# Performance work log

Measured on AMD Instinct MI355X. Metric: run time of the kernel, lower is better.

Reference implementation:

```python
import jax, jax.numpy as jnp
import numpy as np

NUM_HEADS = 16
HEAD_DIM = 64  # hidden 1024 / 16 heads


def setup_inputs() -> dict:
    key = jax.random.key(0)
    ks = jax.random.split(key, 7)
    B, S, D = 16, 1024, 1024
    scale = 1.0 / np.sqrt(D)
    return {
        "hidden_states": jax.random.normal(ks[0], (B, S, D), dtype=jnp.float32),
        "Wq": jax.random.normal(ks[1], (D, D), dtype=jnp.float32) * scale,
        "bq": jax.random.normal(ks[2], (D,), dtype=jnp.float32) * 0.01,
        "Wk": jax.random.normal(ks[3], (D, D), dtype=jnp.float32) * scale,
        "bk": jax.random.normal(ks[4], (D,), dtype=jnp.float32) * 0.01,
        "Wv": jax.random.normal(ks[5], (D, D), dtype=jnp.float32) * scale,
        "bv": jax.random.normal(ks[6], (D,), dtype=jnp.float32) * 0.01,
    }


def _split_heads(x):
    # [B, S, H*Dh] -> [B, H, S, Dh]
    B, S, _ = x.shape
    return x.reshape(B, S, NUM_HEADS, HEAD_DIM).transpose(0, 2, 1, 3)


def reference(hidden_states, Wq, bq, Wk, bk, Wv, bv):
    # Linear layers use torch convention: y = x @ W^T + b
    q = _split_heads(hidden_states @ Wq.T + bq)  # [B,H,S,Dh]
    k = _split_heads(hidden_states @ Wk.T + bk)
    v = _split_heads(hidden_states @ Wv.T + bv)

    scores = jnp.einsum("bhqd,bhkd->bhqk", q, k) / jnp.sqrt(
        jnp.asarray(HEAD_DIM, dtype=q.dtype)
    )
    probs = jax.nn.softmax(scores, axis=-1)  # dropout is identity at eval
    ctx = jnp.einsum("bhqk,bhkd->bhqd", probs, v)  # [B,H,S,Dh]
    B, H, S, Dh = ctx.shape
    return ctx.transpose(0, 2, 1, 3).reshape(B, S, H * Dh)
```

## Files before the change

kernel.cpp:

```cpp
#include <hip/hip_runtime.h>
#include <hip/hip_bf16.h>
#include <cstdint>
#include <math.h>

typedef __bf16 bf16;
typedef __bf16 bf16x8 __attribute__((ext_vector_type(8)));
typedef __bf16 bf16x4 __attribute__((ext_vector_type(4)));
typedef float  f32x4  __attribute__((ext_vector_type(4)));
typedef float  f32x16 __attribute__((ext_vector_type(16)));

#define B_  16
#define S_  1024
#define D_  1024
#define H_  16
#define DH_ 64

__device__ __forceinline__ bf16x8 ld8f(const float* __restrict__ p) {
    f32x4 a = *(const f32x4*)p;
    f32x4 b = *(const f32x4*)(p + 4);
    bf16x8 r;
    r[0] = (bf16)a[0]; r[1] = (bf16)a[1]; r[2] = (bf16)a[2]; r[3] = (bf16)a[3];
    r[4] = (bf16)b[0]; r[5] = (bf16)b[1]; r[6] = (bf16)b[2]; r[7] = (bf16)b[3];
    return r;
}
__device__ __forceinline__ float clampf(float x) {
    return fminf(fmaxf(x, -1e4f), 1e4f);
}
__device__ __forceinline__ void async_ld16(const void* g, void* l) {
    __builtin_amdgcn_global_load_lds(
        (const __attribute__((address_space(1))) void*)(uintptr_t)g,
        (__attribute__((address_space(3))) void*)(uint32_t)(uintptr_t)l,
        16, 0, 0);
}

#define CVT_CHUNKS 2490368u
#define CVT_THREADS 622592u
extern "C" __global__ __launch_bounds__(256)
void cvt_all(const float* __restrict__ X,  const float* __restrict__ Wq,
             const float* __restrict__ Wk, const float* __restrict__ Wv,
             bf16* __restrict__ Xb, bf16* __restrict__ Wb)
{
    const size_t NX = (size_t)B_ * S_ * D_;
    const size_t NW = (size_t)D_ * D_;
    uint32_t tid = blockIdx.x * 256 + threadIdx.x;
    #pragma unroll
    for (int j = 0; j < 4; j++) {
        size_t base = ((size_t)tid + (size_t)j * CVT_THREADS) * 8;
        const float* src; bf16* dst;
        if (base < NX) { src = X + base; dst = Xb + base; }
        else {
            size_t r = base - NX;
            int wsel = (int)(r / NW);
            size_t off = r - (size_t)wsel * NW;
            src = (wsel == 0 ? Wq : (wsel == 1 ? Wk : Wv)) + off;
            dst = Wb + r;
        }
        *(bf16x8*)dst = ld8f(src);
    }
}

extern "C" __global__ __launch_bounds__(512, 2)
void qkv_gemm_bf16(const bf16* __restrict__ Xb, const bf16* __restrict__ Wb,
                   const float* __restrict__ bq, const float* __restrict__ bk,
                   const float* __restrict__ bv,
                   bf16* __restrict__ Qo, bf16* __restrict__ Ko, bf16* __restrict__ Vo)
{
    __shared__ __align__(16) char smem[131072];

    const int t    = threadIdx.x;
    const int w    = t >> 6;
    const int lane = t & 63;
    const int fr   = lane & 15;
    const int fg   = lane >> 4;
    const int wr   = w >> 2;
    const int wn   = w & 3;

    const int id     = blockIdx.x;
    const int l      = id >> 3;
    const int tile_n = l >> 3;
    const int tile_m = (id & 7) * 8 + (l & 7);
    const int m0  = tile_m * 256;
    const int n0  = tile_n * 256;
    const int z   = n0 >> 10;
    const int nz0 = n0 & 1023;

    const bf16* gA = Xb + (size_t)m0 * D_;
    const bf16* gB = Wb + (size_t)n0 * D_;

    auto stage = [&](int kt, uint32_t boff) {
        #pragma unroll
        for (int i = 0; i < 4; i++) {
            uint32_t u   = (uint32_t)(i*512 + w*64 + lane);
            uint32_t row = u >> 3;
            uint32_t c16 = (u & 7u) ^ (row & 7u);
            const bf16* sa = gA + (size_t)row * D_ + kt*64 + c16*8;
            const bf16* sb = gB + (size_t)row * D_ + kt*64 + c16*8;
            async_ld16(sa, smem + boff + (uint32_t)(i*512 + w*64)*16);
            async_ld16(sb, smem + boff + 32768u + (uint32_t)(i*512 + w*64)*16);
        }
    };

    f32x4 acc[8][4];
    #pragma unroll
    for (int i = 0; i < 8; i++)
        #pragma unroll
        for (int j = 0; j < 4; j++) acc[i][j] = (f32x4){0.f,0.f,0.f,0.f};

    stage(0, 0u);
    stage(1, 65536u);
    asm volatile("s_waitcnt vmcnt(8)" ::: "memory");
    __builtin_amdgcn_s_barrier();
    __builtin_amdgcn_sched_barrier(0);

    #pragma unroll 1
    for (int kt = 0; kt < 16; kt++) {
        const uint32_t boff = (uint32_t)(kt & 1) << 16;
        const char* Ab = smem + boff;
        const char* Bb = smem + boff + 32768u;

        #pragma unroll
        for (int kh = 0; kh < 2; kh++) {
            bf16x8 bfr[4];
            #pragma unroll
            for (int ni = 0; ni < 4; ni++) {
                int row = wn*64 + ni*16 + fr;
                bfr[ni] = *(const bf16x8*)(Bb + row*128 +
                             ((((kh<<2)|fg) ^ (fr&7)) << 4));
            }
            #pragma unroll
            for (int mg = 0; mg < 2; mg++) {
                bf16x8 afr[4];
                #pragma unroll
                for (int m4 = 0; m4 < 4; m4++) {
                    int row = wr*128 + (mg*4 + m4)*16 + fr;
                    afr[m4] = *(const bf16x8*)(Ab + row*128 +
                                 ((((kh<<2)|fg) ^ (fr&7)) << 4));
                }
                __builtin_amdgcn_s_setprio(1);
                #pragma unroll
                for (int m4 = 0; m4 < 4; m4++)
                    #pragma unroll
                    for (int ni = 0; ni < 4; ni++)
                        acc[mg*4+m4][ni] = __builtin_amdgcn_mfma_f32_16x16x32_bf16(
                            afr[m4], bfr[ni], acc[mg*4+m4][ni], 0, 0, 0);
                __builtin_amdgcn_s_setprio(0);
            }
        }

        __builtin_amdgcn_s_barrier();
        __builtin_amdgcn_sched_barrier(0);
        if (kt < 14) {
            stage(kt + 2, boff);
            asm volatile("s_waitcnt vmcnt(8)" ::: "memory");
        } else {
            asm volatile("s_waitcnt vmcnt(0)" ::: "memory");
        }
        __builtin_amdgcn_s_barrier();
        __builtin_amdgcn_sched_barrier(0);
    }

    __syncthreads();

    const float* bias = (z == 0) ? bq : ((z == 1) ? bk : bv);
    if (z < 2) {
        bf16* Cs = (bf16*)smem;
        bf16* dst = (z == 0) ? Qo : Ko;
        #pragma unroll
        for (int p = 0; p < 4; p++) {
            if (wr == (p >> 1)) {
                const int mb = (p & 1) * 4;
                #pragma unroll
                for (int ni = 0; ni < 4; ni++) {
                    float bb = bias[nz0 + wn*64 + ni*16 + fr];
                    #pragma unroll
                    for (int m4 = 0; m4 < 4; m4++)
                        #pragma unroll
                        for (int r = 0; r < 4; r++)
                            Cs[(m4*16 + fg*4 + r)*272 + wn*64 + ni*16 + fr] =
                                (bf16)(acc[mb + m4][ni][r] + bb);
                }
            }
            __syncthreads();
            #pragma unroll
            for (int i = 0; i < 4; i++) {
                int c  = t + 512*i;
                int lr = c >> 5, c8 = c & 31;
                int m  = m0 + p*64 + lr;
                int batch = m >> 10, s = m & 1023;
                int ng = nz0 + c8*8;
                int hh = ng >> 6, d0 = ng & 63;
                *(int4*)(dst + (((size_t)(batch*H_ + hh) * S_) + s) * DH_ + d0) =
                    *(const int4*)(Cs + lr*272 + c8*8);
            }
            __syncthreads();
        }
    } else {
        #pragma unroll
        for (int ni = 0; ni < 4; ni++) {
            int nz = nz0 + wn*64 + ni*16 + fr;
            float bb = bias[nz];
            int hh = nz >> 6, d = nz & 63;
            #pragma unroll
            for (int mi = 0; mi < 8; mi++) {
                int m = m0 + wr*128 + mi*16 + fg*4;
                int batch = m >> 10, s = m & 1023;
                bf16x4 pk;
                #pragma unroll
                for (int r = 0; r < 4; r++)
                    pk[r] = (bf16)(acc[mi][ni][r] + bb);
                *(bf16x4*)(Vo + ((size_t)(batch*H_ + hh) * DH_ + d) * S_ + s) = pk;
            }
        }
    }
}

extern "C" __global__ __launch_bounds__(256)
void attn(const bf16* __restrict__ Qw, const bf16* __restrict__ Kw,
          const bf16* __restrict__ Vw, float* __restrict__ out)
{
    __shared__ __align__(16) char KsB[16384];
    __shared__ __align__(16) char VsB[16384];
    __shared__ __align__(16) char PsB[4][2048];

    const int t    = threadIdx.x;
    const int w    = t >> 6;
    const int lane = t & 63;
    const int l31  = lane & 31;
    const int h1   = lane >> 5;

    const int id  = blockIdx.x;
    const int gid = (id & 7) * 256 + (id >> 3);
    const int qt  = gid & 7;
    const int h   = (gid >> 3) & 15;
    const int b   = gid >> 7;

    const bf16* Qh = Qw + (size_t)(b*H_ + h) * S_ * DH_;
    const bf16* Kh = Kw + (size_t)(b*H_ + h) * S_ * DH_;
    const bf16* Vh = Vw + (size_t)(b*H_ + h) * DH_ * S_;

    bf16x8 qf[4];
    {
        const bf16* qp = Qh + (size_t)(qt*128 + w*32 + l31) * DH_ + h1*8;
        #pragma unroll
        for (int ds = 0; ds < 4; ds++)
            qf[ds] = *(const bf16x8*)(qp + ds*16);
    }

    bf16x8 ones;
    #pragma unroll
    for (int i = 0; i < 8; i++) ones[i] = (bf16)1.0f;

    f32x16 acc_o[2], acc_l;
    #pragma unroll
    for (int r = 0; r < 16; r++) { acc_o[0][r] = 0.f; acc_o[1][r] = 0.f; acc_l[r] = 0.f; }

    const float SC_L2E = 0.125f * 1.44269504088896f;
    char* const Pw = PsB[w];

    #pragma unroll 1
    for (int kt = 0; kt < 8; kt++) {
        #pragma unroll
        for (int i = 0; i < 4; i++) {
            int c  = t + 256*i;
            int kr = c >> 3, kc = c & 7;
            int4 kd = *(const int4*)(Kh + (size_t)(kt*128 + kr) * DH_ + kc*8);
            int vr = c >> 4, vc = c & 15;
            int4 vd = *(const int4*)(Vh + (size_t)vr * S_ + kt*128 + vc*8);
            *(int4*)(KsB + kr*128 + ((kc ^ (kr & 7)) << 4)) = kd;
            *(int4*)(VsB + vr*256 + ((vc ^ (vr & 7)) << 4)) = vd;
        }
        __syncthreads();

        #pragma unroll
        for (int ct = 0; ct < 4; ct++) {
            f32x16 sc;
            #pragma unroll
            for (int r = 0; r < 16; r++) sc[r] = 0.f;
            #pragma unroll
            for (int ds = 0; ds < 4; ds++) {
                int kv = ct*32 + l31;
                bf16x8 kf = *(const bf16x8*)(KsB + kv*128 +
                                (((ds*2 + h1) ^ (l31 & 7)) << 4));
                sc = __builtin_amdgcn_mfma_f32_32x32x16_bf16(qf[ds], kf, sc, 0, 0, 0);
            }
            #pragma unroll
            for (int r = 0; r < 16; r++) {
                float p = __builtin_amdgcn_exp2f(sc[r] * SC_L2E);
                int qrow = (r & 3) + 8*(r >> 2) + 4*h1;
                *(bf16*)(Pw + qrow*64 + (((l31 >> 3) ^ (r & 3)) << 4)
                         + (l31 & 7)*2) = (bf16)p;
            }
            #pragma unroll
            for (int ksl = 0; ksl < 2; ksl++) {
                bf16x8 pf = *(const bf16x8*)(Pw + l31*64 +
                                (((ksl*2 + h1) ^ (l31 & 3)) << 4));
                acc_l = __builtin_amdgcn_mfma_f32_32x32x16_bf16(pf, ones, acc_l, 0, 0, 0);
                #pragma unroll
                for (int dt = 0; dt < 2; dt++) {
                    int d  = dt*32 + l31;
                    int ks = ct*2 + ksl;
                    bf16x8 vf = *(const bf16x8*)(VsB + d*256 +
                                    (((ks*2 + h1) ^ (l31 & 7)) << 4));
                    acc_o[dt] = __builtin_amdgcn_mfma_f32_32x32x16_bf16(pf, vf, acc_o[dt], 0, 0, 0);
                }
            }
        }
        __syncthreads();
    }

    #pragma unroll
    for (int r = 0; r < 16; r++) {
        int qrow = (r & 3) + 8*(r >> 2) + 4*h1;
        int s = qt*128 + w*32 + qrow;
        float rl = 1.f / acc_l[r];
        #pragma unroll
        for (int dt = 0; dt < 2; dt++) {
            int d = dt*32 + l31;
            out[((size_t)(b*S_ + s)) * D_ + h*DH_ + d] = acc_o[dt][r] * rl;
        }
    }
}

extern "C" __global__ __launch_bounds__(256)
void qkv_gemm_f32(const float* __restrict__ X,
                  const float* __restrict__ Wq, const float* __restrict__ bq,
                  const float* __restrict__ Wk, const float* __restrict__ bk,
                  const float* __restrict__ Wv, const float* __restrict__ bv,
                  bf16* __restrict__ Qo, bf16* __restrict__ Ko, bf16* __restrict__ Vo)
{
    __shared__ __align__(16) bf16 As[128 * 32];
    __shared__ __align__(16) bf16 Bs[128 * 32];

    const int t    = threadIdx.x;
    const int w    = t >> 6;
    const int lane = t & 63;
    const int fr   = lane & 15;
    const int fg   = lane >> 4;
    const int m0   = blockIdx.x * 128;
    const int n0   = blockIdx.y * 128;
    const int z    = blockIdx.z;

    const float* Wm = (z == 0) ? Wq : ((z == 1) ? Wk : Wv);

    const int wm = (w >> 1) * 64;
    const int wn = (w & 1) * 64;
    const int r0  = t >> 2;
    const int r1  = r0 + 64;
    const int ko0 = (t & 3) * 8;

    f32x4 acc[4][4];
    #pragma unroll
    for (int i = 0; i < 4; i++)
        #pragma unroll
        for (int j = 0; j < 4; j++) acc[i][j] = (f32x4){0.f,0.f,0.f,0.f};

    #pragma unroll 1
    for (int k0 = 0; k0 < D_; k0 += 32) {
        bf16x8 a0 = ld8f(X  + (size_t)(m0 + r0) * D_ + k0 + ko0);
        bf16x8 a1 = ld8f(X  + (size_t)(m0 + r1) * D_ + k0 + ko0);
        bf16x8 b0 = ld8f(Wm + (size_t)(n0 + r0) * D_ + k0 + ko0);
        bf16x8 b1 = ld8f(Wm + (size_t)(n0 + r1) * D_ + k0 + ko0);
        *(bf16x8*)(As + r0 * 32 + ko0) = a0;
        *(bf16x8*)(As + r1 * 32 + ko0) = a1;
        *(bf16x8*)(Bs + r0 * 32 + ko0) = b0;
        *(bf16x8*)(Bs + r1 * 32 + ko0) = b1;
        __syncthreads();

        bf16x8 af[4], bfg[4];
        #pragma unroll
        for (int mi = 0; mi < 4; mi++)
            af[mi] = *(const bf16x8*)(As + (wm + mi*16 + fr) * 32 + fg*8);
        #pragma unroll
        for (int ni = 0; ni < 4; ni++)
            bfg[ni] = *(const bf16x8*)(Bs + (wn + ni*16 + fr) * 32 + fg*8);
        #pragma unroll
        for (int mi = 0; mi < 4; mi++)
            #pragma unroll
            for (int ni = 0; ni < 4; ni++)
                acc[mi][ni] = __builtin_amdgcn_mfma_f32_16x16x32_bf16(
                    af[mi], bfg[ni], acc[mi][ni], 0, 0, 0);
        __syncthreads();
    }

    const float* bias = (z == 0) ? bq : ((z == 1) ? bk : bv);
    if (z < 2) {
        bf16* dst = (z == 0) ? Qo : Ko;
        #pragma unroll
        for (int ni = 0; ni < 4; ni++) {
            int n = n0 + wn + ni*16 + fr;
            float bb = bias[n];
            int hh = n >> 6, d = n & 63;
            #pragma unroll
            for (int mi = 0; mi < 4; mi++)
                #pragma unroll
                for (int r = 0; r < 4; r++) {
                    int m = m0 + wm + mi*16 + fg*4 + r;
                    int batch = m >> 10, s = m & 1023;
                    dst[(((size_t)(batch*H_ + hh) * S_) + s) * DH_ + d] =
                        (bf16)clampf(acc[mi][ni][r] + bb);
                }
        }
    } else {
        #pragma unroll
        for (int ni = 0; ni < 4; ni++) {
            int n = n0 + wn + ni*16 + fr;
            float bb = bias[n];
            int hh = n >> 6, d = n & 63;
            #pragma unroll
            for (int mi = 0; mi < 4; mi++) {
                int m = m0 + wm + mi*16 + fg*4;
                int batch = m >> 10, s = m & 1023;
                bf16x4 pk;
                #pragma unroll
                for (int r = 0; r < 4; r++)
                    pk[r] = (bf16)clampf(acc[mi][ni][r] + bb);
                *(bf16x4*)(Vo + ((size_t)(batch*H_ + hh) * DH_ + d) * S_ + s) = pk;
            }
        }
    }
}

extern "C" __global__ __launch_bounds__(256)
void fused_qkv_attn(const float* __restrict__ X,
                    const float* __restrict__ Wq, const float* __restrict__ bq,
                    const float* __restrict__ Wk, const float* __restrict__ bk,
                    const float* __restrict__ Wv, const float* __restrict__ bv,
                    float* __restrict__ out)
{
    __shared__ __align__(16) char smem[53248];
    bf16* const Qs = (bf16*)smem;
    bf16* const Ks = (bf16*)smem;
    bf16* const Vt = (bf16*)(smem + 18432);
    bf16* const Pp = (bf16*)(smem + 35840) + (threadIdx.x >> 6) * (16 * 136);

    const int t    = threadIdx.x;
    const int w    = t >> 6;
    const int lane = t & 63;
    const int fr   = lane & 15;
    const int fg   = lane >> 4;

    const int qt = blockIdx.x, h = blockIdx.y, b = blockIdx.z;
    const int q0 = qt * 256;

    const float* Xb  = X  + (size_t)b * S_ * D_;
    const float* Wqh = Wq + (size_t)h * DH_ * D_;
    const float* Wkh = Wk + (size_t)h * DH_ * D_;
    const float* Wvh = Wv + (size_t)h * DH_ * D_;

    const float SC_L2E = 0.125f * 1.44269504088896f;
    const float L2E    = 1.44269504088896f;

    {
        f32x4 acc[4][4];
        #pragma unroll
        for (int i = 0; i < 4; i++)
            #pragma unroll
            for (int j = 0; j < 4; j++) acc[i][j] = (f32x4){0.f,0.f,0.f,0.f};
        #pragma unroll 1
        for (int k0 = 0; k0 < D_; k0 += 32) {
            bf16x8 af[4], bw[4];
            #pragma unroll
            for (int mi = 0; mi < 4; mi++)
                af[mi] = ld8f(Xb + (size_t)(q0 + w*64 + mi*16 + fr)*D_ + k0 + fg*8);
            #pragma unroll
            for (int ni = 0; ni < 4; ni++)
                bw[ni] = ld8f(Wqh + (size_t)(ni*16 + fr)*D_ + k0 + fg*8);
            #pragma unroll
            for (int mi = 0; mi < 4; mi++)
                #pragma unroll
                for (int ni = 0; ni < 4; ni++)
                    acc[mi][ni] = __builtin_amdgcn_mfma_f32_16x16x32_bf16(
                        af[mi], bw[ni], acc[mi][ni], 0, 0, 0);
        }
        #pragma unroll
        for (int ni = 0; ni < 4; ni++) {
            float bb = bq[h*DH_ + ni*16 + fr];
            #pragma unroll
            for (int mi = 0; mi < 4; mi++)
                #pragma unroll
                for (int r = 0; r < 4; r++)
                    Qs[(w*64 + mi*16 + fg*4 + r)*72 + ni*16 + fr] =
                        (bf16)clampf(acc[mi][ni][r] + bb);
        }
    }
    __syncthreads();

    bf16x8 qf[4][2];
    #pragma unroll
    for (int mi = 0; mi < 4; mi++)
        #pragma unroll
        for (int ds = 0; ds < 2; ds++)
            qf[mi][ds] = *(const bf16x8*)(Qs + (w*64 + mi*16 + fr)*72 + ds*32 + fg*8);
    __syncthreads();

    float m_run[4][4], l_run[4][4];
    f32x4 acc_o[4][4];
    #pragma unroll
    for (int mi = 0; mi < 4; mi++)
        #pragma unroll
        for (int r = 0; r < 4; r++) { m_run[mi][r] = -1e30f; l_run[mi][r] = 0.f; }
    #pragma unroll
    for (int mi = 0; mi < 4; mi++)
        #pragma unroll
        for (int dt = 0; dt < 4; dt++) acc_o[mi][dt] = (f32x4){0.f,0.f,0.f,0.f};

    #pragma unroll 1
    for (int kt = 0; kt < 8; kt++) {
        {
            f32x4 aK[2][4];
            #pragma unroll
            for (int i = 0; i < 2; i++)
                #pragma unroll
                for (int j = 0; j < 4; j++) aK[i][j] = (f32x4){0.f,0.f,0.f,0.f};
            #pragma unroll 1
            for (int k0 = 0; k0 < D_; k0 += 32) {
                bf16x8 af[2], bw[4];
                #pragma unroll
                for (int mi2 = 0; mi2 < 2; mi2++)
                    af[mi2] = ld8f(Xb + (size_t)(kt*128 + w*32 + mi2*16 + fr)*D_ + k0 + fg*8);
                #pragma unroll
                for (int ni = 0; ni < 4; ni++)
                    bw[ni] = ld8f(Wkh + (size_t)(ni*16 + fr)*D_ + k0 + fg*8);
                #pragma unroll
                for (int mi2 = 0; mi2 < 2; mi2++)
                    #pragma unroll
                    for (int ni = 0; ni < 4; ni++)
                        aK[mi2][ni] = __builtin_amdgcn_mfma_f32_16x16x32_bf16(
                            af[mi2], bw[ni], aK[mi2][ni], 0, 0, 0);
            }
            #pragma unroll
            for (int ni = 0; ni < 4; ni++) {
                float bb = bk[h*DH_ + ni*16 + fr];
                #pragma unroll
                for (int mi2 = 0; mi2 < 2; mi2++)
                    #pragma unroll
                    for (int r = 0; r < 4; r++)
                        Ks[(w*32 + mi2*16 + fg*4 + r)*72 + ni*16 + fr] =
                            (bf16)clampf(aK[mi2][ni][r] + bb);
            }
        }
        {
            f32x4 aV[2][4];
            #pragma unroll
            for (int i = 0; i < 2; i++)
                #pragma unroll
                for (int j = 0; j < 4; j++) aV[i][j] = (f32x4){0.f,0.f,0.f,0.f};
            #pragma unroll 1
            for (int k0 = 0; k0 < D_; k0 += 32) {
                bf16x8 af[2], bw[4];
                #pragma unroll
                for (int mi2 = 0; mi2 < 2; mi2++)
                    af[mi2] = ld8f(Xb + (size_t)(kt*128 + w*32 + mi2*16 + fr)*D_ + k0 + fg*8);
                #pragma unroll
                for (int ni = 0; ni < 4; ni++)
                    bw[ni] = ld8f(Wvh + (size_t)(ni*16 + fr)*D_ + k0 + fg*8);
                #pragma unroll
                for (int mi2 = 0; mi2 < 2; mi2++)
                    #pragma unroll
                    for (int ni = 0; ni < 4; ni++)
                        aV[mi2][ni] = __builtin_amdgcn_mfma_f32_16x16x32_bf16(
                            af[mi2], bw[ni], aV[mi2][ni], 0, 0, 0);
            }
            #pragma unroll
            for (int ni = 0; ni < 4; ni++) {
                float bb = bv[h*DH_ + ni*16 + fr];
                #pragma unroll
                for (int mi2 = 0; mi2 < 2; mi2++)
                    #pragma unroll
                    for (int r = 0; r < 4; r++)
                        Vt[(ni*16 + fr)*136 + w*32 + mi2*16 + fg*4 + r] =
                            (bf16)clampf(aV[mi2][ni][r] + bb);
            }
        }
        __syncthreads();

        #pragma unroll 1
        for (int mi = 0; mi < 4; mi++) {
            f32x4 sc[8];
            #pragma unroll
            for (int ct = 0; ct < 8; ct++) sc[ct] = (f32x4){0.f,0.f,0.f,0.f};
            #pragma unroll
            for (int ct = 0; ct < 8; ct++)
                #pragma unroll
                for (int ds = 0; ds < 2; ds++) {
                    bf16x8 kf = *(const bf16x8*)(Ks + (ct*16 + fr)*72 + ds*32 + fg*8);
                    sc[ct] = __builtin_amdgcn_mfma_f32_16x16x32_bf16(
                        qf[mi][ds], kf, sc[ct], 0, 0, 0);
                }
            #pragma unroll
            for (int ct = 0; ct < 8; ct++)
                #pragma unroll
                for (int r = 0; r < 4; r++)
                    sc[ct][r] = clampf(sc[ct][r]);

            float alpha[4], mneg[4], rsum[4];
            #pragma unroll
            for (int r = 0; r < 4; r++) {
                float mx = sc[0][r];
                #pragma unroll
                for (int ct = 1; ct < 8; ct++) mx = fmaxf(mx, sc[ct][r]);
                #pragma unroll
                for (int off = 8; off >= 1; off >>= 1)
                    mx = fmaxf(mx, __shfl_xor(mx, off));
                float mn = fmaxf(m_run[mi][r], mx * 0.125f);
                alpha[r] = __builtin_amdgcn_exp2f((m_run[mi][r] - mn) * L2E);
                m_run[mi][r] = mn; mneg[r] = mn * L2E; rsum[r] = 0.f;
            }
            #pragma unroll
            for (int ct = 0; ct < 8; ct++)
                #pragma unroll
                for (int r = 0; r < 4; r++) {
                    float p = __builtin_amdgcn_exp2f(sc[ct][r] * SC_L2E - mneg[r]);
                    rsum[r] += p;
                    Pp[(fg*4 + r)*136 + ct*16 + fr] = (bf16)p;
                }
            #pragma unroll
            for (int r = 0; r < 4; r++) {
                float s = rsum[r];
                #pragma unroll
                for (int off = 8; off >= 1; off >>= 1)
                    s += __shfl_xor(s, off);
                l_run[mi][r] = l_run[mi][r] * alpha[r] + s;
            }
            #pragma unroll
            for (int dt = 0; dt < 4; dt++)
                #pragma unroll
                for (int r = 0; r < 4; r++)
                    acc_o[mi][dt][r] *= alpha[r];
            #pragma unroll
            for (int ks = 0; ks < 4; ks++) {
                bf16x8 pf = *(const bf16x8*)(Pp + fr*136 + ks*32 + fg*8);
                #pragma unroll
                for (int dt = 0; dt < 4; dt++) {
                    bf16x8 vf = *(const bf16x8*)(Vt + (dt*16 + fr)*136 + ks*32 + fg*8);
                    acc_o[mi][dt] = __builtin_amdgcn_mfma_f32_16x16x32_bf16(
                        pf, vf, acc_o[mi][dt], 0, 0, 0);
                }
            }
        }
        __syncthreads();
    }

    #pragma unroll
    for (int mi = 0; mi < 4; mi++)
        #pragma unroll
        for (int r = 0; r < 4; r++) {
            float rl = 1.f / l_run[mi][r];
            int s = q0 + w*64 + mi*16 + fg*4 + r;
            #pragma unroll
            for (int dt = 0; dt < 4; dt++) {
                int d = dt*16 + fr;
                out[((size_t)(b*S_ + s)) * D_ + h*DH_ + d] = acc_o[mi][dt][r] * rl;
            }
        }
}

extern "C" void kernel_launch(void* const* d_in, const int* in_sizes, int n_in,
                              void* d_out, int out_size, void* d_ws, size_t ws_size,
                              hipStream_t stream)
{
    const float* X  = (const float*)d_in[0];
    const float* Wq = (const float*)d_in[1];
    const float* bq = (const float*)d_in[2];
    const float* Wk = (const float*)d_in[3];
    const float* bk = (const float*)d_in[4];
    const float* Wv = (const float*)d_in[5];
    const float* bv = (const float*)d_in[6];
    float* outp = (float*)d_out;

    const size_t NX = (size_t)B_ * S_ * D_;
    const size_t NW = (size_t)D_ * D_;
    const size_t needQKV = 3 * NX * sizeof(bf16);
    const size_t need3   = (NX + 3*NW) * sizeof(bf16) + needQKV;

    if (ws_size >= need3) {
        bf16* Xbf = (bf16*)d_ws;
        bf16* Wbf = Xbf + NX;
        bf16* Qw  = Wbf + 3*NW;
        bf16* Kw  = Qw + NX;
        bf16* Vw  = Kw + NX;
        cvt_all<<<dim3(CVT_THREADS / 256), 256, 0, stream>>>(X, Wq, Wk, Wv, Xbf, Wbf);
        qkv_gemm_bf16<<<dim3(768), 512, 0, stream>>>(Xbf, Wbf, bq, bk, bv, Qw, Kw, Vw);
        attn<<<dim3(2048), 256, 0, stream>>>(Qw, Kw, Vw, outp);
    } else if (ws_size >= needQKV) {
        bf16* Qw = (bf16*)d_ws;
        bf16* Kw = Qw + NX;
        bf16* Vw = Kw + NX;
        qkv_gemm_f32<<<dim3(128, 8, 3), 256, 0, stream>>>(X, Wq, bq, Wk, bk, Wv, bv, Qw, Kw, Vw);
        attn<<<dim3(2048), 256, 0, stream>>>(Qw, Kw, Vw, outp);
    } else {
        fused_qkv_attn<<<dim3(4, H_, B_), 256, 0, stream>>>(X, Wq, bq, Wk, bk, Wv, bv, outp);
    }
}
```

Measured before the change: 381.0 us.

## Double-buffer K/V tiles in attention with async global-to-LDS loads

Halves the K/V tile to 64 keys and allocates two LDS buffers, so the next tile is prefetched with async direct-to-LDS loads while the current tile is computed. This is meant to hide global load latency behind the MFMA work instead of stalling at each tile. It also adds a launch bound hint of 4 blocks per CU, which caps register use. Risks include register spills and correctness of the async load visibility, since only one barrier per iteration guards both buffers.

```diff
diff --git a/kernel.cpp b/kernel.cpp
--- a/kernel.cpp
+++ b/kernel.cpp
@@ -214,12 +214,12 @@
     }
 }
 
-extern "C" __global__ __launch_bounds__(256)
+extern "C" __global__ __launch_bounds__(256, 4)
 void attn(const bf16* __restrict__ Qw, const bf16* __restrict__ Kw,
           const bf16* __restrict__ Vw, float* __restrict__ out)
 {
-    __shared__ __align__(16) char KsB[16384];
-    __shared__ __align__(16) char VsB[16384];
+    __shared__ __align__(16) char KsB[2][8192];
+    __shared__ __align__(16) char VsB[2][8192];
     __shared__ __align__(16) char PsB[4][2048];
 
     const int t    = threadIdx.x;
@@ -246,6 +246,19 @@
             qf[ds] = *(const bf16x8*)(qp + ds*16);
     }
 
+    auto stage = [&](int kt, int bsel) {
+        #pragma unroll
+        for (int i = 0; i < 2; i++) {
+            uint32_t u   = (uint32_t)(i*256 + w*64 + lane);
+            uint32_t row = u >> 3;
+            uint32_t c16 = (u & 7u) ^ (row & 7u);
+            async_ld16(Kh + (size_t)(kt*64 + row) * DH_ + c16*8,
+                       &KsB[bsel][(uint32_t)(i*256 + w*64) * 16]);
+            async_ld16(Vh + (size_t)row * S_ + kt*64 + c16*8,
+                       &VsB[bsel][(uint32_t)(i*256 + w*64) * 16]);
+        }
+    };
+
     bf16x8 ones;
     #pragma unroll
     for (int i = 0; i < 8; i++) ones[i] = (bf16)1.0f;
@@ -257,29 +270,26 @@
     const float SC_L2E = 0.125f * 1.44269504088896f;
     char* const Pw = PsB[w];
 
+    stage(0, 0);
+    __syncthreads();
+
     #pragma unroll 1
-    for (int kt = 0; kt < 8; kt++) {
-        #pragma unroll
-        for (int i = 0; i < 4; i++) {
-            int c  = t + 256*i;
-            int kr = c >> 3, kc = c & 7;
-            int4 kd = *(const int4*)(Kh + (size_t)(kt*128 + kr) * DH_ + kc*8);
-            int vr = c >> 4, vc = c & 15;
-            int4 vd = *(const int4*)(Vh + (size_t)vr * S_ + kt*128 + vc*8);
-            *(int4*)(KsB + kr*128 + ((kc ^ (kr & 7)) << 4)) = kd;
-            *(int4*)(VsB + vr*256 + ((vc ^ (vr & 7)) << 4)) = vd;
-        }
-        __syncthreads();
-
-        #pragma unroll
-        for (int ct = 0; ct < 4; ct++) {
+    for (int kt = 0; kt < 16; kt++) {
+        const int bs = kt & 1;
+        if (kt < 15) stage(kt + 1, bs ^ 1);
+
+        const char* Kb = KsB[bs];
+        const char* Vb = VsB[bs];
+
+        #pragma unroll
+        for (int ct = 0; ct < 2; ct++) {
             f32x16 sc;
             #pragma unroll
             for (int r = 0; r < 16; r++) sc[r] = 0.f;
             #pragma unroll
             for (int ds = 0; ds < 4; ds++) {
                 int kv = ct*32 + l31;
-                bf16x8 kf = *(const bf16x8*)(KsB + kv*128 +
+                bf16x8 kf = *(const bf16x8*)(Kb + kv*128 +
                                 (((ds*2 + h1) ^ (l31 & 7)) << 4));
                 sc = __builtin_amdgcn_mfma_f32_32x32x16_bf16(qf[ds], kf, sc, 0, 0, 0);
             }
@@ -299,12 +309,13 @@
                 for (int dt = 0; dt < 2; dt++) {
                     int d  = dt*32 + l31;
                     int ks = ct*2 + ksl;
-                    bf16x8 vf = *(const bf16x8*)(VsB + d*256 +
+                    bf16x8 vf = *(const bf16x8*)(Vb + d*128 +
                                     (((ks*2 + h1) ^ (l31 & 7)) << 4));
                     acc_o[dt] = __builtin_amdgcn_mfma_f32_32x32x16_bf16(pf, vf, acc_o[dt], 0, 0, 0);
                 }
             }
         }
+
         __syncthreads();
     }
 
```

After: 345.7 us. -9.2%, faster.
